# Kernel optimization log

Measured on AMD Instinct MI355X. Metric: run time of the kernel, lower is better.

## Reference

```python
import jax, jax.numpy as jnp
import numpy as np


def _patch_desc(x, patch_size):
    # x: (n, c, h, w). Replicate-pad by patch_size//2 and gather all
    # patch_size*patch_size shifted views -> (n, c*p*p, h*w) descriptors.
    n, c, h, w = x.shape
    step = patch_size // 2
    y = jnp.pad(x, ((0, 0), (0, 0), (step, step), (step, step)), mode='edge')
    feats = [y[:, :, i:i + h, j:j + w]
             for i in range(patch_size) for j in range(patch_size)]
    d = jnp.stack(feats, axis=2)            # (n, c, p*p, h, w)
    return d.reshape(n, c * patch_size * patch_size, h * w)


def setup_inputs() -> dict:
    key = jax.random.key(0)
    k1, k2 = jax.random.split(key)
    n, c, h, w = 4, 16, 64, 64
    s = jax.random.normal(k1, (n, c, h, w), dtype=jnp.float32)
    t = jax.random.normal(k2, (n, c, h, w), dtype=jnp.float32)
    return {"s": s, "t": t, "patch_size": 3}


def reference(s, t, patch_size):
    n, c, h, w = s.shape
    q = _patch_desc(s, patch_size)          # (n, d, hw) source queries
    p = _patch_desc(t, patch_size)          # (n, d, hw) target points
    # Squared-L2 nearest neighbor per source patch (exact version of FLANN kNN)
    qn = jnp.sum(q * q, axis=1)             # (n, hw)
    pn = jnp.sum(p * p, axis=1)             # (n, hw)
    cross = jnp.einsum('ndi,ndj->nij', q, p)  # (n, hw_q, hw_t)
    d2 = qn[:, :, None] - 2.0 * cross + pn[:, None, :]
    idx = jnp.argmin(d2, axis=2)            # (n, hw) flat target index
    nnd = jnp.min(d2, axis=2)               # (n, hw) squared distance
    idy = idx // w
    idx_x = idx % w
    nnf = jnp.stack([idy.reshape(n, h, w), idx_x.reshape(n, h, w)], axis=1)
    nnd = nnd.reshape(n, 1, h, w)
    return nnf.astype(jnp.int32), nnd
```

## Files before the change

### kernel.cpp

```cpp
#include <hip/hip_runtime.h>


#define N_  4
#define C_  16
#define H_  64
#define W_  64
#define HW_ 4096
#define KK_ 18
#define SPLITS_M 4
#define KKSTRIDE 512

#define SPLITS_V 4
#define TILES_PER_SPLIT_V 4

typedef _Float16 f16;
typedef _Float16 f16x8 __attribute__((ext_vector_type(8)));
typedef float    f32x4 __attribute__((ext_vector_type(4)));
typedef float    f32x16 __attribute__((ext_vector_type(16)));

__device__ __forceinline__ int iclamp(int v, int lo, int hi) {
    return v < lo ? lo : (v > hi ? hi : v);
}

__device__ __forceinline__ void async_ld16(const void* g, void* l) {
    __builtin_amdgcn_global_load_lds(
        (const __attribute__((address_space(1))) unsigned int*)g,
        (__attribute__((address_space(3))) unsigned int*)l, 16, 0, 0);
}

__global__ __launch_bounds__(256)
void build_desc_norms_kernel(const float* __restrict__ s,
                             const float* __restrict__ t,
                             f16* __restrict__ Qh, f16* __restrict__ Ql,
                             f16* __restrict__ Ph, f16* __restrict__ Pl,
                             float* __restrict__ pn,
                             float* __restrict__ qn) {
    const int y0  = blockIdx.x;
    const int n   = blockIdx.y;
    const int src = blockIdx.z;
    const float* img = (src ? s : t) + n * (C_ * HW_);
    f16* Dh = src ? Qh : Ph;
    f16* Dl = src ? Ql : Pl;
    float* nrm = src ? qn : pn;

    __shared__ float imgS[3][C_][W_];
    __shared__ float nS[4][W_];
    const int tid = threadIdx.x;
    #pragma unroll
    for (int k = 0; k < 12; ++k) {
        const int idx = tid + k * 256;
        const int x = idx & 63, c = (idx >> 6) & 15, r = idx >> 10;
        const int gy = iclamp(y0 + r - 1, 0, H_ - 1);
        imgS[r][c][x] = img[c * HW_ + gy * W_ + x];
    }
    __syncthreads();

    const int q = tid >> 6, x = tid & 63;
    const int pix = y0 * W_ + x;
    float nacc = 0.f;
    #pragma unroll
    for (int u = 0; u < 5; ++u) {
        const int kk = q * 5 + u;
        if (kk < KK_) {
            f16x8 hv, lv;
            const int d  = kk >> 1;
            const int c0 = (kk & 1) * 8;
            const int dy = (d * 11) >> 5;
            const int dx = d - dy * 3;
            const int xs = iclamp(x + dx - 1, 0, W_ - 1);
            #pragma unroll
            for (int cc = 0; cc < 8; ++cc) {
                const float v = imgS[dy][c0 + cc][xs];
                const f16 h = (f16)v;
                hv[cc] = h;
                lv[cc] = (f16)(v - (float)h);
                nacc += v * v;
            }
            const size_t off = ((size_t)(n * KK_ + kk) * HW_ + pix) * 8;
            *(f16x8*)&Dh[off] = hv;
            *(f16x8*)&Dl[off] = lv;
        }
    }
    nS[q][x] = nacc;
    __syncthreads();
    if (tid < W_)
        nrm[n * HW_ + pix] = nS[0][tid] + nS[1][tid] + nS[2][tid] + nS[3][tid];
}

__global__ __launch_bounds__(256, 2)
void mfma_nn_kernel(const f16* __restrict__ Qh, const f16* __restrict__ Ql,
                    const f16* __restrict__ Ph, const f16* __restrict__ Pl,
                    const float* __restrict__ pn_g,
                    unsigned long long* __restrict__ partial) {
    const int bid   = blockIdx.x;
    const int split = bid & 3;
    const int n     = (bid >> 2) & 3;
    const int iblk  = bid >> 4;
    const int tid  = threadIdx.x;
    const int wave = tid >> 6, lane = tid & 63;
    const int col  = lane & 31;
    const int half = lane >> 5;
    const int irow0 = iblk * 128 + wave * 32;

    __shared__ f16 Bbuf[4][KK_ * KKSTRIDE];
    __shared__ float pnS[1024];

    f16x8 Ah[9], Al[9];
    #pragma unroll
    for (int c = 0; c < 9; ++c) {
        const size_t off = ((size_t)(n * KK_ + 2 * c + half) * HW_ +
                            irow0 + col) * 8;
        Ah[c] = *(const f16x8*)(Qh + off);
        Al[c] = *(const f16x8*)(Ql + off);
    }

    const int jsplit0 = split * 1024;
    #pragma unroll
    for (int k = 0; k < 4; ++k)
        pnS[tid + k * 256] = pn_g[n * HW_ + jsplit0 + tid + k * 256];

    float    bd[16];
    unsigned bj[16];
    #pragma unroll
    for (int r = 0; r < 16; ++r) { bd[r] = -3.0e38f; bj[r] = 0u; }

    const int stile = wave >> 1;
    const int skk0  = (wave & 1) * 9;
    const f16* sbase = half ? Pl : Ph;

    #define STAGE(PAIR, T0)                                                   \
        {   _Pragma("unroll")                                                 \
            for (int u = 0; u < 9; ++u) {                                     \
                const int kk = skk0 + u;                                      \
                const f16* g = sbase + ((size_t)(n * KK_ + kk) * HW_ +        \
                                        jsplit0 + ((T0) + stile) * 32 +       \
                                        col) * 8;                             \
                async_ld16(g, (void*)&Bbuf[(PAIR) * 2 + stile]                \
                                          [kk * KKSTRIDE + lane * 8]);        \
            }                                                                 \
        }

    #define BAR()                                                             \
        {   asm volatile("s_waitcnt vmcnt(0)" ::: "memory");                  \
            asm volatile("s_barrier" ::: "memory");                           \
        }

    #define COMPUTE2(PAIR, T0)                                                \
        {   const int j0 = (T0) * 32 + col;                                   \
            const float pnv0 = -0.5f * pnS[j0];                               \
            const float pnv1 = -0.5f * pnS[j0 + 32];                          \
            f32x16 C0, C1;                                                    \
            _Pragma("unroll")                                                 \
            for (int r = 0; r < 16; ++r) { C0[r] = pnv0; C1[r] = pnv1; }      \
            __builtin_amdgcn_s_setprio(1);                                    \
            _Pragma("unroll")                                                 \
            for (int c = 0; c < 9; ++c) {                                     \
                const int kb = (2 * c + half) * KKSTRIDE + col * 8;           \
                const f16x8 bh0 = *(const f16x8*)&Bbuf[(PAIR) * 2][kb];       \
                const f16x8 bl0 = *(const f16x8*)&Bbuf[(PAIR) * 2][kb + 256]; \
                const f16x8 bh1 = *(const f16x8*)&Bbuf[(PAIR) * 2 + 1][kb];   \
                const f16x8 bl1 = *(const f16x8*)&Bbuf[(PAIR) * 2 + 1]        \
                                                      [kb + 256];             \
                C0 = __builtin_amdgcn_mfma_f32_32x32x16_f16(                  \
                    Ah[c], bh0, C0, 0, 0, 0);                                 \
                C1 = __builtin_amdgcn_mfma_f32_32x32x16_f16(                  \
                    Ah[c], bh1, C1, 0, 0, 0);                                 \
                C0 = __builtin_amdgcn_mfma_f32_32x32x16_f16(                  \
                    Al[c], bh0, C0, 0, 0, 0);                                 \
                C1 = __builtin_amdgcn_mfma_f32_32x32x16_f16(                  \
                    Al[c], bh1, C1, 0, 0, 0);                                 \
                C0 = __builtin_amdgcn_mfma_f32_32x32x16_f16(                  \
                    Ah[c], bl0, C0, 0, 0, 0);                                 \
                C1 = __builtin_amdgcn_mfma_f32_32x32x16_f16(                  \
                    Ah[c], bl1, C1, 0, 0, 0);                                 \
            }                                                                 \
            __builtin_amdgcn_s_setprio(0);                                    \
            _Pragma("unroll")                                                 \
            for (int r = 0; r < 16; ++r) {                                    \
                if (C0[r] > bd[r]) { bd[r] = C0[r]; bj[r] = (unsigned)j0; }   \
                if (C1[r] > bd[r]) { bd[r] = C1[r];                           \
                                     bj[r] = (unsigned)(j0 + 32); }           \
            }                                                                 \
        }

    STAGE(0, 0)
    asm volatile("s_waitcnt vmcnt(0)" ::: "memory");
    __syncthreads();

    STAGE(1, 2)  COMPUTE2(0, 0)
    for (int gg = 0; gg < 6; ++gg) {
        const int t4 = gg * 4;
        BAR()  STAGE(0, t4 + 4)  COMPUTE2(1, t4 + 2)
        BAR()  STAGE(1, t4 + 6)  COMPUTE2(0, t4 + 4)
    }
    BAR()  STAGE(0, 28)  COMPUTE2(1, 26)
    BAR()  STAGE(1, 30)  COMPUTE2(0, 28)
    BAR()               COMPUTE2(1, 30)
    #undef STAGE
    #undef BAR
    #undef COMPUTE2

    #pragma unroll
    for (int r = 0; r < 16; ++r) {
        float    d = bd[r];
        unsigned j = (unsigned)jsplit0 + bj[r];
        #pragma unroll
        for (int off = 1; off < 32; off <<= 1) {
            const float    od = __shfl_xor(d, off, 64);
            const unsigned oj = __shfl_xor(j, off, 64);
            const bool take = (od > d) || (od == d && oj < j);
            d = take ? od : d;
            j = take ? oj : j;
        }
        if (col == 0) {
            const int i = irow0 + (r & 3) + 8 * (r >> 2) + 4 * half;
            partial[(size_t)(split * N_ + n) * HW_ + i] =
                ((unsigned long long)j << 32) |
                (unsigned long long)__float_as_uint(-2.f * d);
        }
    }
}

__global__ __launch_bounds__(256)
void finalize_mfma_kernel(const unsigned long long* __restrict__ partial,
                          const float* __restrict__ qn_g,
                          float* __restrict__ out) {
    const int id  = blockIdx.x * 256 + threadIdx.x;
    const int n   = id >> 12;
    const int pix = id & 4095;
    float    bd = 3.0e38f;
    unsigned bj = 0u;
    #pragma unroll
    for (int sp = 0; sp < SPLITS_M; ++sp) {
        const unsigned long long v = partial[(size_t)(sp * N_ + n) * HW_ + pix];
        const float    d = __uint_as_float((unsigned)(v & 0xffffffffull));
        const unsigned j = (unsigned)(v >> 32);
        const bool take = (d < bd) || (d == bd && j < bj);
        bd = take ? d : bd;
        bj = take ? j : bj;
    }
    out[n * 2 * HW_ + pix]            = (float)(bj >> 6);
    out[n * 2 * HW_ + HW_ + pix]      = (float)(bj & 63);
    out[N_ * 2 * HW_ + n * HW_ + pix] = bd + qn_g[n * HW_ + pix];
}

__global__ __launch_bounds__(256)
void prep_norms_kernel(const float* __restrict__ s,
                       const float* __restrict__ t,
                       float* __restrict__ pn,
                       float* __restrict__ qn) {
    const int gid   = blockIdx.x * 256 + threadIdx.x;
    const int which = gid >> 14;
    const int id    = gid & 16383;
    const int n     = id >> 12;
    const int pix   = id & 4095;
    const int y = pix >> 6, x = pix & 63;
    const float* base = (which ? s : t) + n * (C_ * HW_);
    float acc = 0.f;
    for (int c = 0; c < C_; ++c) {
        const float* bc = base + c * HW_;
        #pragma unroll
        for (int dy = 0; dy < 3; ++dy) {
            const float* br = bc + iclamp(y + dy - 1, 0, H_ - 1) * W_;
            #pragma unroll
            for (int dx = 0; dx < 3; ++dx) {
                float v = br[iclamp(x + dx - 1, 0, W_ - 1)];
                acc += v * v;
            }
        }
    }
    (which ? qn : pn)[id] = acc;
}

__global__ __launch_bounds__(256)
void patchmatch_main_kernel(const float* __restrict__ s,
                            const float* __restrict__ t,
                            const float* __restrict__ pn_g,
                            const float* __restrict__ qn_g,
                            unsigned long long* __restrict__ partial) {
    const int yq    = blockIdx.x;
    const int n     = blockIdx.y;
    const int split = blockIdx.z;
    const int tid  = threadIdx.x;
    const int tx   = tid & 15;
    const int ty   = tid >> 4;
    const int i0   = ty * 4;
    const int jrow = tx >> 2;
    const int jx0  = (tx & 3) * 16;

    __shared__ float qS[C_][3][68];
    __shared__ float tS[C_][6][68];
    __shared__ float qnS[W_];

    const float* sb = s + n * (C_ * HW_);
    const float* tb = t + n * (C_ * HW_);

    #pragma unroll
    for (int k = 0; k < 3; ++k) {
        const int id = tid + k * 256;
        const int sg = id & 15;
        const int c  = (id >> 4) & 15;
        const int r  = id >> 8;
        const int gr = iclamp(yq + r - 1, 0, H_ - 1);
        const float4 v = *(const float4*)&sb[c * HW_ + gr * W_ + sg * 4];
        float* dst = &qS[c][r][1 + sg * 4];
        dst[0] = v.x; dst[1] = v.y; dst[2] = v.z; dst[3] = v.w;
    }
    if (tid < 48) {
        const int c  = tid & 15;
        const int r  = tid >> 4;
        const int gr = iclamp(yq + r - 1, 0, H_ - 1);
        qS[c][r][0]  = sb[c * HW_ + gr * W_];
        qS[c][r][65] = sb[c * HW_ + gr * W_ + 63];
    }
    if (tid < W_) qnS[tid] = qn_g[n * HW_ + yq * W_ + tid];

    unsigned long long best[4] = {~0ull, ~0ull, ~0ull, ~0ull};

    for (int ytl = 0; ytl < TILES_PER_SPLIT_V; ++ytl) {
        const int yt = split * TILES_PER_SPLIT_V + ytl;
        __syncthreads();
        #pragma unroll
        for (int k = 0; k < 6; ++k) {
            const int id = tid + k * 256;
            const int sg = id & 15;
            const int c  = (id >> 4) & 15;
            const int r  = id >> 8;
            const int gr = iclamp(4 * yt + r - 1, 0, H_ - 1);
            const float4 v = *(const float4*)&tb[c * HW_ + gr * W_ + sg * 4];
            float* dst = &tS[c][r][1 + sg * 4];
            dst[0] = v.x; dst[1] = v.y; dst[2] = v.z; dst[3] = v.w;
        }
        if (tid < 96) {
            const int c  = tid & 15;
            const int r  = tid >> 4;
            const int gr = iclamp(4 * yt + r - 1, 0, H_ - 1);
            tS[c][r][0]  = tb[c * HW_ + gr * W_];
            tS[c][r][65] = tb[c * HW_ + gr * W_ + 63];
        }
        __syncthreads();

        float acc[4][16];
        #pragma unroll
        for (int a = 0; a < 4; ++a)
            #pragma unroll
            for (int b = 0; b < 16; ++b) acc[a][b] = 0.f;

        for (int c = 0; c < C_; ++c) {
            #pragma unroll
            for (int dy = 0; dy < 3; ++dy) {
                float qv[6], tv[18];
                *(float4*)&qv[0] = *(const float4*)&qS[c][dy][i0];
                *(float2*)&qv[4] = *(const float2*)&qS[c][dy][i0 + 4];
                const float* trow = &tS[c][jrow + dy][jx0];
                *(float4*)&tv[0]  = *(const float4*)&trow[0];
                *(float4*)&tv[4]  = *(const float4*)&trow[4];
                *(float4*)&tv[8]  = *(const float4*)&trow[8];
                *(float4*)&tv[12] = *(const float4*)&trow[12];
                *(float2*)&tv[16] = *(const float2*)&trow[16];
                #pragma unroll
                for (int dx = 0; dx < 3; ++dx)
                    #pragma unroll
                    for (int a = 0; a < 4; ++a)
                        #pragma unroll
                        for (int b = 0; b < 16; ++b)
                            acc[a][b] += qv[a + dx] * tv[b + dx];
            }
        }

        const int jbase = yt * 256 + jrow * W_ + jx0;
        float pnv[16];
        const float* png = &pn_g[n * HW_ + jbase];
        *(float4*)&pnv[0]  = *(const float4*)&png[0];
        *(float4*)&pnv[4]  = *(const float4*)&png[4];
        *(float4*)&pnv[8]  = *(const float4*)&png[8];
        *(float4*)&pnv[12] = *(const float4*)&png[12];
        #pragma unroll
        for (int a = 0; a < 4; ++a) {
            const float qn = qnS[i0 + a];
            #pragma unroll
            for (int b = 0; b < 16; ++b) {
                const float d2 = qn + pnv[b] - 2.f * acc[a][b];
                unsigned long long cand =
                    ((unsigned long long)__float_as_uint(d2) << 32) |
                    (unsigned)(jbase + b);
                best[a] = cand < best[a] ? cand : best[a];
            }
        }
    }

    #pragma unroll
    for (int a = 0; a < 4; ++a) {
        unsigned long long v = best[a];
        #pragma unroll
        for (int mm = 8; mm >= 1; mm >>= 1) {
            unsigned long long o = __shfl_xor(v, mm, 64);
            v = o < v ? o : v;
        }
        best[a] = v;
    }
    if (tx == 0) {
        #pragma unroll
        for (int a = 0; a < 4; ++a)
            partial[((split * N_ + n) * HW_) + yq * W_ + i0 + a] = best[a];
    }
}

__global__ __launch_bounds__(256)
void finalize_kernel(const unsigned long long* __restrict__ partial,
                     float* __restrict__ out) {
    const int id  = blockIdx.x * 256 + threadIdx.x;
    const int n   = id >> 12;
    const int pix = id & 4095;
    unsigned long long best = ~0ull;
    #pragma unroll
    for (int sp = 0; sp < SPLITS_V; ++sp) {
        unsigned long long v = partial[(sp * N_ + n) * HW_ + pix];
        best = v < best ? v : best;
    }
    const unsigned j = (unsigned)(best & 0xffffffffu);
    const float d2 = __uint_as_float((unsigned)(best >> 32));
    out[n * 2 * HW_ + pix]            = (float)(j >> 6);
    out[n * 2 * HW_ + HW_ + pix]      = (float)(j & 63);
    out[N_ * 2 * HW_ + n * HW_ + pix] = d2;
}

__global__ __launch_bounds__(256)
void patchmatch_mono_kernel(const float* __restrict__ s,
                            const float* __restrict__ t,
                            float* __restrict__ out) {
    const int yq  = blockIdx.x;
    const int n   = blockIdx.y;
    const int tid = threadIdx.x;
    const int tx  = tid & 15;
    const int ty  = tid >> 4;
    const int i0  = ty * 4;
    const int jrow = tx >> 3;
    const int jx0  = (tx & 7) * 8;

    __shared__ float qS[C_][3][68];
    __shared__ float tS[C_][4][68];
    __shared__ float pnS[HW_];
    __shared__ float qnS[W_];

    const float* sb = s + n * (C_ * HW_);
    const float* tb = t + n * (C_ * HW_);

    for (int jj = tid; jj < HW_; jj += 256) {
        const int y = jj >> 6, x = jj & 63;
        float acc = 0.f;
        for (int c = 0; c < C_; ++c) {
            const float* tc = tb + c * HW_;
            #pragma unroll
            for (int dy = 0; dy < 3; ++dy) {
                const float* tr = tc + iclamp(y + dy - 1, 0, H_ - 1) * W_;
                #pragma unroll
                for (int dx = 0; dx < 3; ++dx) {
                    float v = tr[iclamp(x + dx - 1, 0, W_ - 1)];
                    acc += v * v;
                }
            }
        }
        pnS[jj] = acc;
    }
    for (int idx = tid; idx < C_ * 3 * 66; idx += 256) {
        const int c   = idx / (3 * 66);
        const int rem = idx - c * (3 * 66);
        const int rr  = rem / 66;
        const int xi  = rem - rr * 66;
        qS[c][rr][xi] = sb[c * HW_ + iclamp(yq + rr - 1, 0, H_ - 1) * W_ +
                           iclamp(xi - 1, 0, W_ - 1)];
    }
    __syncthreads();
    if (tid < W_) {
        float acc = 0.f;
        for (int c = 0; c < C_; ++c)
            #pragma unroll
            for (int dy = 0; dy < 3; ++dy)
                #pragma unroll
                for (int dx = 0; dx < 3; ++dx) {
                    float v = qS[c][dy][tid + dx];
                    acc += v * v;
                }
        qnS[tid] = acc;
    }

    unsigned long long best[4] = {~0ull, ~0ull, ~0ull, ~0ull};
    for (int yt = 0; yt < 32; ++yt) {
        __syncthreads();
        for (int idx = tid; idx < C_ * 4 * 66; idx += 256) {
            const int c   = idx / (4 * 66);
            const int rem = idx - c * (4 * 66);
            const int rr  = rem / 66;
            const int xi  = rem - rr * 66;
            tS[c][rr][xi] = tb[c * HW_ + iclamp(2 * yt + rr - 1, 0, H_ - 1) * W_ +
                               iclamp(xi - 1, 0, W_ - 1)];
        }
        __syncthreads();

        float acc[4][8];
        #pragma unroll
        for (int a = 0; a < 4; ++a)
            #pragma unroll
            for (int b = 0; b < 8; ++b) acc[a][b] = 0.f;

        for (int c = 0; c < C_; ++c) {
            #pragma unroll
            for (int dy = 0; dy < 3; ++dy) {
                float qv[8], tv[12];
                *(float4*)&qv[0] = *(const float4*)&qS[c][dy][i0];
                *(float4*)&qv[4] = *(const float4*)&qS[c][dy][i0 + 4];
                const float* trow = &tS[c][jrow + dy][jx0];
                *(float4*)&tv[0] = *(const float4*)&trow[0];
                *(float4*)&tv[4] = *(const float4*)&trow[4];
                *(float4*)&tv[8] = *(const float4*)&trow[8];
                #pragma unroll
                for (int dx = 0; dx < 3; ++dx)
                    #pragma unroll
                    for (int a = 0; a < 4; ++a)
                        #pragma unroll
                        for (int b = 0; b < 8; ++b)
                            acc[a][b] += qv[a + dx] * tv[b + dx];
            }
        }
        const int rbase = (2 * yt + jrow) * W_ + jx0;
        #pragma unroll
        for (int a = 0; a < 4; ++a) {
            const float qn = qnS[i0 + a];
            #pragma unroll
            for (int b = 0; b < 8; ++b) {
                const int j = rbase + b;
                const float d2 = qn + pnS[j] - 2.f * acc[a][b];
                unsigned long long cand =
                    ((unsigned long long)__float_as_uint(d2) << 32) | (unsigned)j;
                best[a] = cand < best[a] ? cand : best[a];
            }
        }
    }
    #pragma unroll
    for (int a = 0; a < 4; ++a) {
        unsigned long long v = best[a];
        #pragma unroll
        for (int mm = 8; mm >= 1; mm >>= 1) {
            unsigned long long o = __shfl_xor(v, mm, 64);
            v = o < v ? o : v;
        }
        best[a] = v;
    }
    if (tx == 0) {
        #pragma unroll
        for (int a = 0; a < 4; ++a) {
            const int x = i0 + a;
            const unsigned j = (unsigned)(best[a] & 0xffffffffu);
            const float d2 = __uint_as_float((unsigned)(best[a] >> 32));
            const int pix = yq * W_ + x;
            out[n * 2 * HW_ + pix]            = (float)(j >> 6);
            out[n * 2 * HW_ + HW_ + pix]      = (float)(j & 63);
            out[N_ * 2 * HW_ + n * HW_ + pix] = d2;
        }
    }
}

extern "C" void kernel_launch(void* const* d_in, const int* in_sizes, int n_in,
                              void* d_out, int out_size, void* d_ws, size_t ws_size,
                              hipStream_t stream) {
    const float* s = (const float*)d_in[0];
    const float* t = (const float*)d_in[1];
    float* out = (float*)d_out;

    const size_t norm_b  = (size_t)N_ * HW_ * 4;
    const size_t part_b  = (size_t)SPLITS_M * N_ * HW_ * 8;
    const size_t desc_b  = (size_t)N_ * HW_ * KK_ * 8 * 2;
    const size_t need_m  = 2 * norm_b + part_b + 4 * desc_b;

    if (ws_size >= need_m) {
        char* w = (char*)d_ws;
        float* pn = (float*)w;                       w += norm_b;
        float* qn = (float*)w;                       w += norm_b;
        unsigned long long* partial = (unsigned long long*)w; w += part_b;
        f16* Qh = (f16*)w;  w += desc_b;
        f16* Ql = (f16*)w;  w += desc_b;
        f16* Ph = (f16*)w;  w += desc_b;
        f16* Pl = (f16*)w;

        build_desc_norms_kernel<<<dim3(64, N_, 2), 256, 0, stream>>>(
            s, t, Qh, Ql, Ph, Pl, pn, qn);
        mfma_nn_kernel<<<512, 256, 0, stream>>>(Qh, Ql, Ph, Pl, pn, partial);
        finalize_mfma_kernel<<<64, 256, 0, stream>>>(partial, qn, out);
        return;
    }

    const size_t need_v = 2 * norm_b + (size_t)SPLITS_V * N_ * HW_ * 8;
    if (ws_size >= need_v) {
        float* pn = (float*)d_ws;
        float* qn = pn + N_ * HW_;
        unsigned long long* partial =
            (unsigned long long*)((char*)d_ws + 2 * norm_b);
        prep_norms_kernel<<<128, 256, 0, stream>>>(s, t, pn, qn);
        dim3 grid(H_, N_, SPLITS_V);
        patchmatch_main_kernel<<<grid, 256, 0, stream>>>(s, t, pn, qn, partial);
        finalize_kernel<<<64, 256, 0, stream>>>(partial, out);
        return;
    }

    dim3 grid(H_, N_);
    patchmatch_mono_kernel<<<grid, 256, 0, stream>>>(s, t, out);
}
```

Before: 124.4 us.

## Fuse split-K finalize into NN kernel via atomicMin and last-block counter

Removes the separate finalize kernel. Each block now merges its per-row best (distance, index) into one global array using atomicMin on an order-preserving 64-bit key. The last block per row tile, detected with an atomic counter, decodes the result and writes the output. Two memsets are added to initialise the best array and the counters, and the descriptor-build image load is vectorised to float4. This trades one kernel launch and the partial-buffer round trip for atomics and two memset operations.

```diff
diff --git a/kernel.cpp b/kernel.cpp
--- a/kernel.cpp
+++ b/kernel.cpp
@@ -47,11 +47,12 @@
     __shared__ float nS[4][W_];
     const int tid = threadIdx.x;
     #pragma unroll
-    for (int k = 0; k < 12; ++k) {
-        const int idx = tid + k * 256;
-        const int x = idx & 63, c = (idx >> 6) & 15, r = idx >> 10;
+    for (int k = 0; k < 3; ++k) {
+        const int i4 = tid + k * 256;
+        const int x4 = i4 & 15, c = (i4 >> 4) & 15, r = i4 >> 8;
         const int gy = iclamp(y0 + r - 1, 0, H_ - 1);
-        imgS[r][c][x] = img[c * HW_ + gy * W_ + x];
+        const float4 v = *(const float4*)&img[c * HW_ + gy * W_ + x4 * 4];
+        *(float4*)&imgS[r][c][x4 * 4] = v;
     }
     __syncthreads();
 
@@ -91,7 +92,10 @@
 void mfma_nn_kernel(const f16* __restrict__ Qh, const f16* __restrict__ Ql,
                     const f16* __restrict__ Ph, const f16* __restrict__ Pl,
                     const float* __restrict__ pn_g,
-                    unsigned long long* __restrict__ partial) {
+                    const float* __restrict__ qn_g,
+                    unsigned long long* __restrict__ best,
+                    unsigned* __restrict__ cnt,
+                    float* __restrict__ out) {
     const int bid   = blockIdx.x;
     const int split = bid & 3;
     const int n     = (bid >> 2) & 3;
@@ -102,8 +106,9 @@
     const int half = lane >> 5;
     const int irow0 = iblk * 128 + wave * 32;
 
-    __shared__ f16 Bbuf[4][KK_ * KKSTRIDE];
+    __shared__ __align__(16) f16 Bbuf[4][KK_ * KKSTRIDE];
     __shared__ float pnS[1024];
+    __shared__ int lastFlag;
 
     f16x8 Ah[9], Al[9];
     #pragma unroll
@@ -214,34 +219,34 @@
         }
         if (col == 0) {
             const int i = irow0 + (r & 3) + 8 * (r >> 2) + 4 * half;
-            partial[(size_t)(split * N_ + n) * HW_ + i] =
-                ((unsigned long long)j << 32) |
-                (unsigned long long)__float_as_uint(-2.f * d);
-        }
-    }
-}
-
-__global__ __launch_bounds__(256)
-void finalize_mfma_kernel(const unsigned long long* __restrict__ partial,
-                          const float* __restrict__ qn_g,
-                          float* __restrict__ out) {
-    const int id  = blockIdx.x * 256 + threadIdx.x;
-    const int n   = id >> 12;
-    const int pix = id & 4095;
-    float    bd = 3.0e38f;
-    unsigned bj = 0u;
-    #pragma unroll
-    for (int sp = 0; sp < SPLITS_M; ++sp) {
-        const unsigned long long v = partial[(size_t)(sp * N_ + n) * HW_ + pix];
-        const float    d = __uint_as_float((unsigned)(v & 0xffffffffull));
-        const unsigned j = (unsigned)(v >> 32);
-        const bool take = (d < bd) || (d == bd && j < bj);
-        bd = take ? d : bd;
-        bj = take ? j : bj;
-    }
-    out[n * 2 * HW_ + pix]            = (float)(bj >> 6);
-    out[n * 2 * HW_ + HW_ + pix]      = (float)(bj & 63);
-    out[N_ * 2 * HW_ + n * HW_ + pix] = bd + qn_g[n * HW_ + pix];
+            unsigned ub = __float_as_uint(-2.f * d);
+            ub = (ub & 0x80000000u) ? ~ub : (ub | 0x80000000u);
+            const unsigned long long key =
+                ((unsigned long long)ub << 32) | (unsigned long long)j;
+            atomicMin(&best[(size_t)n * HW_ + i], key);
+        }
+    }
+
+    __syncthreads();
+    if (tid == 0) {
+        __threadfence();
+        const unsigned old = atomicAdd(&cnt[n * 32 + iblk], 1u);
+        lastFlag = (old == SPLITS_M - 1);
+    }
+    __syncthreads();
+
+    if (lastFlag && half == 0) {
+        const int i = irow0 + col;
+        const size_t gi = (size_t)n * HW_ + i;
+        const unsigned long long v = atomicOr(&best[gi], 0ull);
+        const unsigned j = (unsigned)(v & 0xffffffffu);
+        unsigned ub = (unsigned)(v >> 32);
+        ub = (ub & 0x80000000u) ? (ub & 0x7fffffffu) : ~ub;
+        out[(size_t)n * 2 * HW_ + i]       = (float)(j >> 6);
+        out[(size_t)n * 2 * HW_ + HW_ + i] = (float)(j & 63);
+        out[(size_t)N_ * 2 * HW_ + gi]     =
+            __uint_as_float(ub) + qn_g[gi];
+    }
 }
 
 __global__ __launch_bounds__(256)
@@ -568,25 +573,29 @@
     const float* t = (const float*)d_in[1];
     float* out = (float*)d_out;
 
-    const size_t norm_b  = (size_t)N_ * HW_ * 4;
-    const size_t part_b  = (size_t)SPLITS_M * N_ * HW_ * 8;
-    const size_t desc_b  = (size_t)N_ * HW_ * KK_ * 8 * 2;
-    const size_t need_m  = 2 * norm_b + part_b + 4 * desc_b;
+    const size_t norm_b = (size_t)N_ * HW_ * 4;
+    const size_t best_b = (size_t)N_ * HW_ * 8;
+    const size_t cnt_b  = 4096;
+    const size_t desc_b = (size_t)N_ * HW_ * KK_ * 8 * 2;
+    const size_t need_m = 2 * norm_b + best_b + cnt_b + 4 * desc_b;
 
     if (ws_size >= need_m) {
         char* w = (char*)d_ws;
         float* pn = (float*)w;                       w += norm_b;
         float* qn = (float*)w;                       w += norm_b;
-        unsigned long long* partial = (unsigned long long*)w; w += part_b;
+        unsigned long long* best = (unsigned long long*)w; w += best_b;
+        unsigned* cnt = (unsigned*)w;                w += cnt_b;
         f16* Qh = (f16*)w;  w += desc_b;
         f16* Ql = (f16*)w;  w += desc_b;
         f16* Ph = (f16*)w;  w += desc_b;
         f16* Pl = (f16*)w;
 
+        hipMemsetAsync(best, 0xFF, best_b, stream);
+        hipMemsetAsync(cnt, 0, (size_t)N_ * 32 * 4, stream);
         build_desc_norms_kernel<<<dim3(64, N_, 2), 256, 0, stream>>>(
             s, t, Qh, Ql, Ph, Pl, pn, qn);
-        mfma_nn_kernel<<<512, 256, 0, stream>>>(Qh, Ql, Ph, Pl, pn, partial);
-        finalize_mfma_kernel<<<64, 256, 0, stream>>>(partial, qn, out);
+        mfma_nn_kernel<<<512, 256, 0, stream>>>(
+            Qh, Ql, Ph, Pl, pn, qn, best, cnt, out);
         return;
     }
 
```

Result: slower. 130.3 us (+4.8%).
